# Kernel optimization log

Measured on AMD Instinct MI355X. Metric: run time of the kernel, lower is better.

The kernel has to match this reference:

```python
import jax, jax.numpy as jnp
import numpy as np

B, D, NS, C, H = 4096, 1024, 16000, 1000, 256


def setup_inputs() -> dict:
    key = jax.random.key(0)
    ks = jax.random.split(key, 8)
    # L2-normalized image features (output of frozen CLIP encode_image + norm)
    q = jax.random.normal(ks[0], (B, D), jnp.float32)
    q = q / jnp.linalg.norm(q, axis=-1, keepdims=True)
    # zero-shot CLIP logits
    z = jax.random.normal(ks[1], (B, C), jnp.float32)
    # L2-normalized support/cache features
    keys = jax.random.normal(ks[2], (NS, D), jnp.float32)
    keys = keys / jnp.linalg.norm(keys, axis=-1, keepdims=True)
    # one-hot support labels
    labels = jax.random.randint(ks[3], (NS,), 0, C)
    values = jax.nn.one_hot(labels, C, dtype=jnp.float32)
    # gate MLP params (small init like nn.Linear default scale)
    fc1_w = jax.random.normal(ks[4], (H, D), jnp.float32) * 0.02
    fc1_b = jnp.zeros((H,), jnp.float32)
    fc2_w = jax.random.normal(ks[5], (2, H), jnp.float32) * 0.02
    fc2_b = jnp.zeros((2,), jnp.float32)
    post_scale = jnp.ones((1,), jnp.float32)
    return {"q": q, "z": z, "keys": keys, "values": values,
            "fc1_w": fc1_w, "fc1_b": fc1_b, "fc2_w": fc2_w, "fc2_b": fc2_b,
            "post_scale": post_scale}


def reference(q, z, keys, values, fc1_w, fc1_b, fc2_w, fc2_b, post_scale):
    # GateMLP: per-image alpha in (0,1), beta > 0
    x = jax.nn.relu(q @ fc1_w.T + fc1_b)            # [B, H]
    g = x @ fc2_w.T + fc2_b                          # [B, 2]
    alpha_hat = jax.nn.sigmoid(g[:, 0:1])            # [B, 1]
    beta = jax.nn.softplus(g[:, 1:2]) + 0.001        # [B, 1] (learn_beta=True)
    # cache logits: sim -> exp affinity -> label aggregation
    sim = q @ keys.T                                 # [B, Ns]
    affinity = jnp.exp(beta * sim)                   # [B, Ns]
    c = affinity @ values                            # [B, C]
    # gated convex fusion with zero-shot logits
    logits = ((1.0 - alpha_hat) * z + alpha_hat * c) * post_scale
    return (logits, alpha_hat, beta)
```

## Files before the change

kernel.cpp:

```cpp
#include <hip/hip_runtime.h>
#include <hip/hip_bf16.h>
#include <stdint.h>

#define B_  4096
#define D_  1024
#define NS_ 16000
#define C_  1000
#define H_  256
#define LBLK 4000
#define RSTRIDE 2048

typedef __attribute__((ext_vector_type(8))) short bf16x8;
typedef __attribute__((ext_vector_type(4))) float f32x4;
typedef __attribute__((ext_vector_type(16))) float f32x16;
typedef __attribute__((ext_vector_type(8))) int i32x8;

__device__ __forceinline__ unsigned short f2bf(float f) {
  union { float f; unsigned u; } v; v.f = f;
  unsigned u = v.u;
  u += 0x7FFF + ((u >> 16) & 1);
  return (unsigned short)(u >> 16);
}

__device__ __forceinline__ float bf2f(unsigned short h) {
  union { unsigned u; float f; } v; v.u = ((unsigned)h) << 16;
  return v.f;
}

__global__ void prep_kernel(const float4* __restrict__ q, const float4* __restrict__ keys,
                            const float4* __restrict__ fc1, const float* __restrict__ values,
                            ushort4* __restrict__ qb, int* __restrict__ q8,
                            int* __restrict__ keys8, ushort4* __restrict__ fc1b,
                            int* __restrict__ labels, int* __restrict__ hist) {
  if (blockIdx.x < LBLK) {
    const int s = blockIdx.x * 4 + (threadIdx.x >> 6);
    const int lane = threadIdx.x & 63;
    const float4* row = (const float4*)(values + (size_t)s * C_);
    int lab = -1;
    for (int j = lane; j < C_ / 4; j += 64) {
      float4 v = row[j];
      if (v.x > 0.5f) lab = j * 4 + 0;
      if (v.y > 0.5f) lab = j * 4 + 1;
      if (v.z > 0.5f) lab = j * 4 + 2;
      if (v.w > 0.5f) lab = j * 4 + 3;
      if (__ballot(lab >= 0)) break;
    }
    if (lab >= 0) { labels[s] = lab; atomicAdd(&hist[lab], 1); }
    return;
  }
  const int cb = blockIdx.x - LBLK;
  if (cb < 512) {
    const size_t n = (size_t)B_ * D_ / 4;
    for (size_t i = (size_t)cb * 256 + threadIdx.x; i < n; i += 512 * 256) {
      float4 v = q[i];
      ushort4 r; r.x = f2bf(v.x); r.y = f2bf(v.y); r.z = f2bf(v.z); r.w = f2bf(v.w);
      qb[i] = r;
      int p = __builtin_amdgcn_cvt_pk_fp8_f32(v.x * 64.f, v.y * 64.f, 0, false);
      p     = __builtin_amdgcn_cvt_pk_fp8_f32(v.z * 64.f, v.w * 64.f, p, true);
      q8[i] = p;
    }
  } else if (cb < 2560) {
    const size_t n = (size_t)NS_ * D_ / 4;
    for (size_t i = (size_t)(cb - 512) * 256 + threadIdx.x; i < n; i += 2048 * 256) {
      float4 v = keys[i];
      int p = __builtin_amdgcn_cvt_pk_fp8_f32(v.x * 64.f, v.y * 64.f, 0, false);
      p     = __builtin_amdgcn_cvt_pk_fp8_f32(v.z * 64.f, v.w * 64.f, p, true);
      keys8[i] = p;
    }
  } else {
    const size_t n = (size_t)H_ * D_ / 4;
    for (size_t i = (size_t)(cb - 2560) * 256 + threadIdx.x; i < n; i += 32 * 256) {
      float4 v = fc1[i];
      ushort4 r; r.x = f2bf(v.x); r.y = f2bf(v.y); r.z = f2bf(v.z); r.w = f2bf(v.w);
      fc1b[i] = r;
    }
  }
}

__global__ __launch_bounds__(1024) void sortpipe_kernel(
    const int* __restrict__ hist, const int* __restrict__ labels,
    int* __restrict__ sortidx, int* __restrict__ runid, int* __restrict__ labstart)
{
  __shared__ int sscan[1024];
  __shared__ int sboff[C_ + 1];
  __shared__ int scnt[C_];
  __shared__ unsigned short slab[NS_];
  __shared__ int stile[NS_ / 128];
  const int t = threadIdx.x;

  int v = (t < C_) ? hist[t] : 0;
  sscan[t] = v;
  if (t < C_) scnt[t] = 0;
  __syncthreads();
  for (int off = 1; off < 1024; off <<= 1) {
    int u = (t >= off) ? sscan[t - off] : 0;
    __syncthreads(); sscan[t] += u; __syncthreads();
  }
  if (t == 0) sboff[0] = 0;
  if (t < C_) sboff[t + 1] = sscan[t];
  __syncthreads();

  for (int s = t; s < NS_; s += 1024) {
    const int lab = labels[s];
    const int pos = sboff[lab] + atomicAdd(&scnt[lab], 1);
    sortidx[pos] = s;
    slab[pos] = (unsigned short)lab;
  }
  __syncthreads();

  const int c0 = t * 16;
  int flags[16]; int cnt = 0;
  if (c0 < NS_) {
    int prev = (c0 == 0) ? slab[0] : slab[c0 - 1];
    #pragma unroll
    for (int i = 0; i < 16; ++i) {
      const int l = slab[c0 + i];
      const int f = ((c0 + i) != 0) && (l != prev);
      flags[i] = f; cnt += f; prev = l;
    }
  }
  sscan[t] = cnt; __syncthreads();
  for (int off = 1; off < 1024; off <<= 1) {
    int u = (t >= off) ? sscan[t - off] : 0;
    __syncthreads(); sscan[t] += u; __syncthreads();
  }
  if (c0 < NS_ && (t & 7) == 0) stile[t >> 3] = (sscan[t] - cnt) + flags[0];
  __syncthreads();
  if (c0 < NS_) {
    int run = sscan[t] - cnt;
    const int base = (c0 >> 7) * 16 - stile[c0 >> 7];
    #pragma unroll
    for (int i = 0; i < 16; ++i) {
      run += flags[i];
      runid[c0 + i] = base + run;
    }
  }
  if (t == 0) runid[NS_] = (NS_ >> 7) * 16;
  __threadfence();
  __syncthreads();
  if (t <= C_) labstart[t] = runid[sboff[t]];
}

__global__ __launch_bounds__(256, 2) void gemmgate_kernel(
    const short* __restrict__ A, const short* __restrict__ Bm,
    const float* __restrict__ bias, const float* __restrict__ fc2_w,
    const float* __restrict__ fc2_b, float* __restrict__ ab)
{
  __shared__ short As[32 * 64];
  __shared__ short Bs[256 * 64];
  __shared__ float gred[4][32][2];

  const int tid  = threadIdx.x;
  const int wave = tid >> 6, lane = tid & 63;
  const int quad = lane >> 4, l16 = lane & 15;
  const int wn = wave;
  const int rstart = blockIdx.x * 32;

  f32x4 acc[2][4];
  #pragma unroll
  for (int i = 0; i < 2; ++i)
    #pragma unroll
    for (int j = 0; j < 4; ++j) acc[i][j] = (f32x4)0.f;

  const int r_  = (lane >> 3);
  const int kc_ = ((lane & 7) ^ r_) * 8;

  for (int kt = 0; kt < D_; kt += 64) {
    __syncthreads();
    {
      const int row = wave * 8 + r_;
      const short* gA = A + (size_t)(rstart + row) * D_ + kt + kc_;
      __builtin_amdgcn_global_load_lds(
          (const __attribute__((address_space(1))) void*)gA,
          (__attribute__((address_space(3))) void*)(As + wave * 512), 16, 0, 0);
    }
    #pragma unroll
    for (int i = 0; i < 8; ++i) {
      const int g = i * 4 + wave;
      const int row = g * 8 + r_;
      const short* gB = Bm + (size_t)row * D_ + kt + kc_;
      __builtin_amdgcn_global_load_lds(
          (const __attribute__((address_space(1))) void*)gB,
          (__attribute__((address_space(3))) void*)(Bs + g * 512), 16, 0, 0);
    }
    __syncthreads();
    #pragma unroll
    for (int ks = 0; ks < 64; ks += 32) {
      bf16x8 af[2], bfr[4];
      const int kb = (ks >> 3) + quad;
      #pragma unroll
      for (int mt = 0; mt < 2; ++mt) {
        const int row = mt * 16 + l16;
        af[mt] = *(const bf16x8*)(As + row * 64 + ((kb ^ (row & 7)) << 3));
      }
      #pragma unroll
      for (int nt = 0; nt < 4; ++nt) {
        const int row = wn * 64 + nt * 16 + l16;
        bfr[nt] = *(const bf16x8*)(Bs + row * 64 + ((kb ^ (row & 7)) << 3));
      }
      #pragma unroll
      for (int mt = 0; mt < 2; ++mt)
        #pragma unroll
        for (int nt = 0; nt < 4; ++nt)
          acc[mt][nt] = __builtin_amdgcn_mfma_f32_16x16x32_bf16(af[mt], bfr[nt], acc[mt][nt], 0, 0, 0);
    }
  }

  float g0p[2][4], g1p[2][4];
  #pragma unroll
  for (int mt = 0; mt < 2; ++mt)
    #pragma unroll
    for (int r = 0; r < 4; ++r) { g0p[mt][r] = 0.f; g1p[mt][r] = 0.f; }
  #pragma unroll
  for (int nt = 0; nt < 4; ++nt) {
    const int col = wn * 64 + nt * 16 + l16;
    const float bv = bias[col];
    const float w0 = fc2_w[col], w1 = fc2_w[H_ + col];
    #pragma unroll
    for (int mt = 0; mt < 2; ++mt)
      #pragma unroll
      for (int r = 0; r < 4; ++r) {
        float xv = acc[mt][nt][r] + bv;
        xv = xv > 0.f ? xv : 0.f;
        g0p[mt][r] += xv * w0;
        g1p[mt][r] += xv * w1;
      }
  }
  #pragma unroll
  for (int mt = 0; mt < 2; ++mt)
    #pragma unroll
    for (int r = 0; r < 4; ++r) {
      float a0 = g0p[mt][r], a1 = g1p[mt][r];
      #pragma unroll
      for (int off = 8; off > 0; off >>= 1) {
        a0 += __shfl_xor(a0, off);
        a1 += __shfl_xor(a1, off);
      }
      if (l16 == 0) {
        const int row = mt * 16 + quad * 4 + r;
        gred[wave][row][0] = a0;
        gred[wave][row][1] = a1;
      }
    }
  __syncthreads();
  if (tid < 32) {
    float g0 = gred[0][tid][0] + gred[1][tid][0] + gred[2][tid][0] + gred[3][tid][0] + fc2_b[0];
    float g1 = gred[0][tid][1] + gred[1][tid][1] + gred[2][tid][1] + gred[3][tid][1] + fc2_b[1];
    ab[rstart + tid]      = 1.f / (1.f + __expf(-g0));
    ab[B_ + rstart + tid] = fmaxf(g1, 0.f) + log1pf(__expf(-fabsf(g1))) + 0.001f;
  }
}

__device__ __forceinline__ i32x8 mx_frag(const char* base, int lrow, int kh, int sel) {
  const int c0 = kh * 4 + sel * 2;
  const int s = lrow & 7;
  const int4 lo = *(const int4*)(base + lrow * 128 + (((c0    ) ^ s) << 4));
  const int4 hi = *(const int4*)(base + lrow * 128 + (((c0 + 1) ^ s) << 4));
  i32x8 f;
  f[0] = lo.x; f[1] = lo.y; f[2] = lo.z; f[3] = lo.w;
  f[4] = hi.x; f[5] = hi.y; f[6] = hi.z; f[7] = hi.w;
  return f;
}

__global__ __launch_bounds__(256, 2) void mxgemm_kernel(
    const char* __restrict__ A8, const char* __restrict__ B8,
    const float* __restrict__ beta, float* __restrict__ partials,
    const int* __restrict__ sortidx, const int* __restrict__ runid)
{
  __shared__ __align__(16) char smem[32768];
  __shared__ float sbeta[128];
  __shared__ __align__(16) unsigned short Es[16 * 136];
  char* As = smem;
  char* Bs = smem + 16384;

  const int tid  = threadIdx.x;
  const int wave = tid >> 6, lane = tid & 63;
  const int sel  = lane >> 5, l32 = lane & 31;
  const int wm = wave >> 1, wn = wave & 1;
  const int rstart = blockIdx.x * 128;
  const int nstart = blockIdx.y * 128;

  for (int i = tid; i < (16 * 136) / 2; i += 256) ((int*)Es)[i] = 0;
  if (tid < 128) sbeta[tid] = beta[rstart + tid];
  __syncthreads();
  if (tid < 128) Es[(runid[nstart + tid] & 15) * 136 + tid] = 0x3F80;

  const int srow_ = (lane >> 3);
  const int gch_  = (lane & 7) ^ srow_;

  int arow[4], brow[4];
  #pragma unroll
  for (int i = 0; i < 4; ++i) {
    const int row = wave * 32 + i * 8 + srow_;
    arow[i] = rstart + row;
    brow[i] = sortidx[nstart + row];
  }

  f32x16 acc[2][2];
  #pragma unroll
  for (int i = 0; i < 2; ++i)
    #pragma unroll
    for (int j = 0; j < 2; ++j) acc[i][j] = (f32x16)0.f;

  for (int kt = 0; kt < D_; kt += 128) {
    __syncthreads();
    #pragma unroll
    for (int i = 0; i < 4; ++i) {
      const char* gA = A8 + (size_t)arow[i] * D_ + kt + (gch_ << 4);
      const char* gB = B8 + (size_t)brow[i] * D_ + kt + (gch_ << 4);
      __builtin_amdgcn_global_load_lds(
          (const __attribute__((address_space(1))) void*)gA,
          (__attribute__((address_space(3))) void*)(As + wave * 4096 + i * 1024), 16, 0, 0);
      __builtin_amdgcn_global_load_lds(
          (const __attribute__((address_space(1))) void*)gB,
          (__attribute__((address_space(3))) void*)(Bs + wave * 4096 + i * 1024), 16, 0, 0);
    }
    __syncthreads();
    #pragma unroll
    for (int kh = 0; kh < 2; ++kh) {
      i32x8 a0 = mx_frag(As, wm * 64 +  0 + l32, kh, sel);
      i32x8 a1 = mx_frag(As, wm * 64 + 32 + l32, kh, sel);
      i32x8 b0 = mx_frag(Bs, wn * 64 +  0 + l32, kh, sel);
      i32x8 b1 = mx_frag(Bs, wn * 64 + 32 + l32, kh, sel);
      acc[0][0] = __builtin_amdgcn_mfma_scale_f32_32x32x64_f8f6f4(a0, b0, acc[0][0], 0, 0, 0, 121, 0, 121);
      acc[0][1] = __builtin_amdgcn_mfma_scale_f32_32x32x64_f8f6f4(a0, b1, acc[0][1], 0, 0, 0, 121, 0, 121);
      acc[1][0] = __builtin_amdgcn_mfma_scale_f32_32x32x64_f8f6f4(a1, b0, acc[1][0], 0, 0, 0, 121, 0, 121);
      acc[1][1] = __builtin_amdgcn_mfma_scale_f32_32x32x64_f8f6f4(a1, b1, acc[1][1], 0, 0, 0, 121, 0, 121);
    }
  }

  __syncthreads();
  unsigned short* tile = (unsigned short*)smem;
  #pragma unroll
  for (int mt = 0; mt < 2; ++mt) {
    #pragma unroll
    for (int nt = 0; nt < 2; ++nt) {
      const int col = wn * 64 + nt * 32 + l32;
      const int cc = col >> 3, cl = col & 7;
      #pragma unroll
      for (int r = 0; r < 16; ++r) {
        const int row = wm * 64 + mt * 32 + (r & 3) + 8 * (r >> 2) + 4 * sel;
        const float v = __expf(sbeta[row] * acc[mt][nt][r]);
        tile[row * 128 + (((cc ^ (row & 7)) << 3) | cl)] = f2bf(v);
      }
    }
  }
  __syncthreads();

  {
    const int quad = lane >> 4, l16 = lane & 15;
    const int rowb = wave * 32;
    f32x4 racc[2];
    racc[0] = (f32x4)0.f; racc[1] = (f32x4)0.f;
    #pragma unroll
    for (int kc = 0; kc < 4; ++kc) {
      const bf16x8 bfrag = *(const bf16x8*)(Es + l16 * 136 + kc * 32 + quad * 8);
      #pragma unroll
      for (int rg = 0; rg < 2; ++rg) {
        const int row = rowb + rg * 16 + l16;
        const int kch = kc * 4 + quad;
        const bf16x8 afrag = *(const bf16x8*)(tile + row * 128 + ((kch ^ (row & 7)) << 3));
        racc[rg] = __builtin_amdgcn_mfma_f32_16x16x32_bf16(afrag, bfrag, racc[rg], 0, 0, 0);
      }
    }
    const int tb = (nstart >> 7) * 16;
    #pragma unroll
    for (int rg = 0; rg < 2; ++rg) {
      #pragma unroll
      for (int r = 0; r < 4; ++r) {
        const int row = rowb + rg * 16 + quad * 4 + r;
        partials[(size_t)(rstart + row) * RSTRIDE + tb + l16] = racc[rg][r];
      }
    }
  }
}

__global__ __launch_bounds__(256) void reduce_kernel(
    const float* __restrict__ partials, const int* __restrict__ labstart,
    const float* __restrict__ z, const float* __restrict__ ps, float* __restrict__ out) {
  __shared__ float sp[RSTRIDE];
  __shared__ int sls[C_ + 1];
  const int b = blockIdx.x;
  const int t = threadIdx.x;
  for (int i = t; i <= C_; i += 256) sls[i] = labstart[i];
  __syncthreads();
  const int R = sls[C_];
  const float* prow = partials + (size_t)b * RSTRIDE;
  for (int i = t; i < R; i += 256) sp[i] = prow[i];
  __syncthreads();
  const float a  = out[(size_t)B_ * C_ + b];
  const float sc = ps[0];
  for (int lab = t; lab < C_; lab += 256) {
    float c = 0.f;
    for (int j = sls[lab]; j < sls[lab + 1]; ++j) c += sp[j];
    const size_t oi = (size_t)b * C_ + lab;
    out[oi] = ((1.f - a) * z[oi] + a * c) * sc;
  }
}

extern "C" void kernel_launch(void* const* d_in, const int* in_sizes, int n_in,
                              void* d_out, int out_size, void* d_ws, size_t ws_size,
                              hipStream_t stream) {
  const float* q          = (const float*)d_in[0];
  const float* z          = (const float*)d_in[1];
  const float* keys       = (const float*)d_in[2];
  const float* values     = (const float*)d_in[3];
  const float* fc1_w      = (const float*)d_in[4];
  const float* fc1_b      = (const float*)d_in[5];
  const float* fc2_w      = (const float*)d_in[6];
  const float* fc2_b      = (const float*)d_in[7];
  const float* post_scale = (const float*)d_in[8];
  float* out = (float*)d_out;

  char* ws = (char*)d_ws;
  short* qb        = (short*)(ws);
  char*  q8        = (char*) (ws +  8388608);
  char*  keys8     = (char*) (ws + 12582912);
  short* fc1b      = (short*)(ws + 28966912);
  int*   labels    = (int*)  (ws + 29491200);
  int*   hist      = (int*)  (ws + 33749504);
  int*   sortidx   = (int*)  (ws + 33761792);
  int*   runid     = (int*)  (ws + 33889792);
  int*   labstart  = (int*)  (ws + 33953808);
  float* partials  = (float*)(ws + 33959936);

  float* alpha = out + (size_t)B_ * C_;
  float* beta  = alpha + B_;

  hipMemsetAsync(hist, 0, 4096, stream);

  prep_kernel<<<LBLK + 2592, 256, 0, stream>>>(
      (const float4*)q, (const float4*)keys, (const float4*)fc1_w, values,
      (ushort4*)qb, (int*)q8, (int*)keys8, (ushort4*)fc1b, labels, hist);

  sortpipe_kernel<<<1, 1024, 0, stream>>>(hist, labels, sortidx, runid, labstart);

  gemmgate_kernel<<<B_ / 32, 256, 0, stream>>>(qb, fc1b, fc1_b, fc2_w, fc2_b, alpha);

  mxgemm_kernel<<<dim3(B_ / 128, NS_ / 128), 256, 0, stream>>>(
      q8, keys8, beta, partials, sortidx, runid);

  reduce_kernel<<<B_, 256, 0, stream>>>(partials, labstart, z, post_scale, out);
}
```

Measured before the change: 328.6 us.

## Restructure prep block mapping, swizzle GEMM tile order, vectorize reduce loads

The prep kernel now gives each block a fixed four-element chunk of conversion work, replacing grid-stride loops, and runs the conversion blocks before the label-scan blocks. The FP8 GEMM switches to a 1D grid whose block index is remapped so that blocks scheduled close together, likely spread across XCDs, share key tiles, with the aim of improving cache reuse. The reduce kernel copies the full partial row with float4 loads and drops one barrier. It now always reads all RSTRIDE entries instead of only the used ones, which adds some extra traffic.

Measured after the change: 324.3 us. No clear change (-1.3%).

```diff
diff --git a/kernel.cpp b/kernel.cpp
--- a/kernel.cpp
+++ b/kernel.cpp
@@ -8,6 +8,10 @@
 #define C_  1000
 #define H_  256
 #define LBLK 4000
+#define QCB  1024
+#define KCB  4000
+#define FCB  64
+#define CONVB (QCB + KCB + FCB)
 #define RSTRIDE 2048
 
 typedef __attribute__((ext_vector_type(8))) short bf16x8;
@@ -32,26 +36,12 @@
                             ushort4* __restrict__ qb, int* __restrict__ q8,
                             int* __restrict__ keys8, ushort4* __restrict__ fc1b,
                             int* __restrict__ labels, int* __restrict__ hist) {
-  if (blockIdx.x < LBLK) {
-    const int s = blockIdx.x * 4 + (threadIdx.x >> 6);
-    const int lane = threadIdx.x & 63;
-    const float4* row = (const float4*)(values + (size_t)s * C_);
-    int lab = -1;
-    for (int j = lane; j < C_ / 4; j += 64) {
-      float4 v = row[j];
-      if (v.x > 0.5f) lab = j * 4 + 0;
-      if (v.y > 0.5f) lab = j * 4 + 1;
-      if (v.z > 0.5f) lab = j * 4 + 2;
-      if (v.w > 0.5f) lab = j * 4 + 3;
-      if (__ballot(lab >= 0)) break;
-    }
-    if (lab >= 0) { labels[s] = lab; atomicAdd(&hist[lab], 1); }
-    return;
-  }
-  const int cb = blockIdx.x - LBLK;
-  if (cb < 512) {
-    const size_t n = (size_t)B_ * D_ / 4;
-    for (size_t i = (size_t)cb * 256 + threadIdx.x; i < n; i += 512 * 256) {
+  const int bid = blockIdx.x;
+  if (bid < QCB) {
+    const size_t i0 = (size_t)bid * 1024 + threadIdx.x;
+    #pragma unroll
+    for (int k = 0; k < 4; ++k) {
+      const size_t i = i0 + k * 256;
       float4 v = q[i];
       ushort4 r; r.x = f2bf(v.x); r.y = f2bf(v.y); r.z = f2bf(v.z); r.w = f2bf(v.w);
       qb[i] = r;
@@ -59,22 +49,44 @@
       p     = __builtin_amdgcn_cvt_pk_fp8_f32(v.z * 64.f, v.w * 64.f, p, true);
       q8[i] = p;
     }
-  } else if (cb < 2560) {
-    const size_t n = (size_t)NS_ * D_ / 4;
-    for (size_t i = (size_t)(cb - 512) * 256 + threadIdx.x; i < n; i += 2048 * 256) {
+    return;
+  }
+  if (bid < QCB + KCB) {
+    const size_t i0 = (size_t)(bid - QCB) * 1024 + threadIdx.x;
+    #pragma unroll
+    for (int k = 0; k < 4; ++k) {
+      const size_t i = i0 + k * 256;
       float4 v = keys[i];
       int p = __builtin_amdgcn_cvt_pk_fp8_f32(v.x * 64.f, v.y * 64.f, 0, false);
       p     = __builtin_amdgcn_cvt_pk_fp8_f32(v.z * 64.f, v.w * 64.f, p, true);
       keys8[i] = p;
     }
-  } else {
-    const size_t n = (size_t)H_ * D_ / 4;
-    for (size_t i = (size_t)(cb - 2560) * 256 + threadIdx.x; i < n; i += 32 * 256) {
+    return;
+  }
+  if (bid < CONVB) {
+    const size_t i0 = (size_t)(bid - QCB - KCB) * 1024 + threadIdx.x;
+    #pragma unroll
+    for (int k = 0; k < 4; ++k) {
+      const size_t i = i0 + k * 256;
       float4 v = fc1[i];
       ushort4 r; r.x = f2bf(v.x); r.y = f2bf(v.y); r.z = f2bf(v.z); r.w = f2bf(v.w);
       fc1b[i] = r;
     }
-  }
+    return;
+  }
+  const int s = (bid - CONVB) * 4 + (threadIdx.x >> 6);
+  const int lane = threadIdx.x & 63;
+  const float4* row = (const float4*)(values + (size_t)s * C_);
+  int lab = -1;
+  for (int j = lane; j < C_ / 4; j += 64) {
+    float4 v = row[j];
+    if (v.x > 0.5f) lab = j * 4 + 0;
+    if (v.y > 0.5f) lab = j * 4 + 1;
+    if (v.z > 0.5f) lab = j * 4 + 2;
+    if (v.w > 0.5f) lab = j * 4 + 3;
+    if (__ballot(lab >= 0)) break;
+  }
+  if (lab >= 0) { labels[s] = lab; atomicAdd(&hist[lab], 1); }
 }
 
 __global__ __launch_bounds__(1024) void sortpipe_kernel(
@@ -277,8 +289,10 @@
   const int wave = tid >> 6, lane = tid & 63;
   const int sel  = lane >> 5, l32 = lane & 31;
   const int wm = wave >> 1, wn = wave & 1;
-  const int rstart = blockIdx.x * 128;
-  const int nstart = blockIdx.y * 128;
+
+  const int sb  = (blockIdx.x & 7) * 500 + (blockIdx.x >> 3);
+  const int rstart = (sb & 31) * 128;
+  const int nstart = (sb >> 5) * 128;
 
   for (int i = tid; i < (16 * 136) / 2; i += 256) ((int*)Es)[i] = 0;
   if (tid < 128) sbeta[tid] = beta[rstart + tid];
@@ -378,15 +392,14 @@
 __global__ __launch_bounds__(256) void reduce_kernel(
     const float* __restrict__ partials, const int* __restrict__ labstart,
     const float* __restrict__ z, const float* __restrict__ ps, float* __restrict__ out) {
-  __shared__ float sp[RSTRIDE];
+  __shared__ __align__(16) float sp[RSTRIDE];
   __shared__ int sls[C_ + 1];
   const int b = blockIdx.x;
   const int t = threadIdx.x;
   for (int i = t; i <= C_; i += 256) sls[i] = labstart[i];
-  __syncthreads();
-  const int R = sls[C_];
-  const float* prow = partials + (size_t)b * RSTRIDE;
-  for (int i = t; i < R; i += 256) sp[i] = prow[i];
+  const float4* p4 = (const float4*)(partials + (size_t)b * RSTRIDE);
+  float4* s4 = (float4*)sp;
+  for (int i = t; i < RSTRIDE / 4; i += 256) s4[i] = p4[i];
   __syncthreads();
   const float a  = out[(size_t)B_ * C_ + b];
   const float sc = ps[0];
@@ -429,7 +442,7 @@
 
   hipMemsetAsync(hist, 0, 4096, stream);
 
-  prep_kernel<<<LBLK + 2592, 256, 0, stream>>>(
+  prep_kernel<<<CONVB + LBLK, 256, 0, stream>>>(
       (const float4*)q, (const float4*)keys, (const float4*)fc1_w, values,
       (ushort4*)qb, (int*)q8, (int*)keys8, (ushort4*)fc1b, labels, hist);
 
@@ -437,7 +450,7 @@
 
   gemmgate_kernel<<<B_ / 32, 256, 0, stream>>>(qb, fc1b, fc1_b, fc2_w, fc2_b, alpha);
 
-  mxgemm_kernel<<<dim3(B_ / 128, NS_ / 128), 256, 0, stream>>>(
+  mxgemm_kernel<<<4000, 256, 0, stream>>>(
       q8, keys8, beta, partials, sortidx, runid);
 
   reduce_kernel<<<B_, 256, 0, stream>>>(partials, labstart, z, post_scale, out);
```
